# Performance work log

Measured on AMD Instinct MI355X. Metric: run time of the kernel, lower is better.

## Reference

```python
import jax, jax.numpy as jnp
import numpy as np

N_NODES = 100000
N_EDGES = 1600000
IN_DIM = 128
OUT_DIM = 32
N_HEADS = 4
NEG_SLOPE = 0.2  # DGL GATConv default LeakyReLU negative slope


def setup_inputs() -> dict:
    key = jax.random.key(0)
    k_h, k_src, k_dst, k_w, k_al, k_ar = jax.random.split(key, 6)
    h = jax.random.normal(k_h, (N_NODES, IN_DIM), dtype=jnp.float32)
    src = jax.random.randint(k_src, (N_EDGES,), 0, N_NODES, dtype=jnp.int32)
    dst = jnp.sort(jax.random.randint(k_dst, (N_EDGES,), 0, N_NODES, dtype=jnp.int32))
    # Xavier-ish init scale
    W = jax.random.normal(k_w, (IN_DIM, N_HEADS * OUT_DIM), dtype=jnp.float32) / np.sqrt(IN_DIM)
    attn_l = jax.random.normal(k_al, (N_HEADS, OUT_DIM), dtype=jnp.float32) / np.sqrt(OUT_DIM)
    attn_r = jax.random.normal(k_ar, (N_HEADS, OUT_DIM), dtype=jnp.float32) / np.sqrt(OUT_DIM)
    bias = jnp.zeros((N_HEADS * OUT_DIM,), dtype=jnp.float32)
    return {"h": h, "src": src, "dst": dst, "W": W, "attn_l": attn_l, "attn_r": attn_r, "bias": bias}


def reference(h, src, dst, W, attn_l, attn_r, bias):
    # Eval-mode GATConv (feat_drop / attn_drop disabled).
    N = h.shape[0]
    # Linear projection -> [N, H, D]
    feat = (h @ W).reshape(N, N_HEADS, OUT_DIM)
    # Per-node attention logits: el/er [N, H]
    el = jnp.einsum('nhd,hd->nh', feat, attn_l)
    er = jnp.einsum('nhd,hd->nh', feat, attn_r)
    # Edge scores: e = LeakyReLU(el[src] + er[dst])  -> [E, H]
    e = el[src] + er[dst]
    e = jnp.where(e > 0, e, NEG_SLOPE * e)
    # Segment softmax over incoming edges of each destination node
    e_max = jax.ops.segment_max(e, dst, num_segments=N, indices_are_sorted=True)
    e_exp = jnp.exp(e - e_max[dst])
    denom = jax.ops.segment_sum(e_exp, dst, num_segments=N, indices_are_sorted=True)
    alpha = e_exp / denom[dst]  # [E, H]
    # Weighted aggregate: sum_e alpha[e] * feat[src[e]] per destination
    msg = feat[src] * alpha[:, :, None]  # [E, H, D]
    rst = jax.ops.segment_sum(msg, dst, num_segments=N, indices_are_sorted=True)  # [N, H, D]
    # Bias + ReLU activation (GATLayer default activation=F.relu)
    rst = rst + bias.reshape(1, N_HEADS, OUT_DIM)
    return jax.nn.relu(rst)
```

## Files before the change

### kernel.cpp

```cpp
#include <hip/hip_runtime.h>
#include <hip/hip_fp16.h>
#include <math.h>

#define NEG_SLOPE 0.2f

typedef _Float16 f16x2 __attribute__((ext_vector_type(2)));
typedef _Float16 f16x8 __attribute__((ext_vector_type(8)));
typedef float f32x4 __attribute__((ext_vector_type(4)));

__device__ __forceinline__ float fdot2f(unsigned int a, unsigned int b, float c) {
#if __has_builtin(__builtin_amdgcn_fdot2)
    return __builtin_amdgcn_fdot2(__builtin_bit_cast(f16x2, a),
                                  __builtin_bit_cast(f16x2, b), c, false);
#else
    __half2 ah = __builtin_bit_cast(__half2, a), bh = __builtin_bit_cast(__half2, b);
    float2 af = __half22float2(ah), bf = __half22float2(bh);
    return c + af.x * bf.x + af.y * bf.y;
#endif
}

__device__ __forceinline__ unsigned int packw(float a, float b) {
#if __has_builtin(__builtin_amdgcn_cvt_pkrtz)
    return __builtin_bit_cast(unsigned int, __builtin_amdgcn_cvt_pkrtz(a, b));
#else
    return __builtin_bit_cast(unsigned int, __floats2half2_rn(a, b));
#endif
}

__global__ __launch_bounds__(256) void prep_seg_kernel(
    const float* __restrict__ W, __half* __restrict__ w16t,
    const int* __restrict__ dst, int* __restrict__ off, int E, int N)
{
    const int b = blockIdx.x;
    if (b < 64) {
        int tid = b * 256 + threadIdx.x;
        int c = tid >> 7, k = tid & 127;
        w16t[c * 128 + k] = __float2half(W[k * 128 + c]);
        return;
    }
    int i = (b - 64) * 256 + threadIdx.x;
    if (i >= E) return;
    int d = dst[i];
    int prev = (i == 0) ? -1 : dst[i - 1];
    for (int n = prev + 1; n <= d; ++n) off[n] = i;
    if (i == E - 1) {
        for (int n = d + 1; n <= N; ++n) off[n] = E;
    }
}

__global__ __launch_bounds__(256) void proj_kernel(
    const float* __restrict__ h, const __half* __restrict__ w16t,
    const float* __restrict__ attn_l, const float* __restrict__ attn_r,
    __half* __restrict__ feat, float* __restrict__ el, float* __restrict__ er,
    int N)
{
    __shared__ __half hl[64 * 128];
    __shared__ __half wl[128 * 128];
    const int t = threadIdx.x;
    const int nodeBase = blockIdx.x * 64;

#pragma unroll
    for (int i = 0; i < 8; ++i) {
        int ch = t + i * 256;
        int col = ch >> 4, k8 = ch & 15;
        uint4 v = *(const uint4*)(w16t + col * 128 + k8 * 8);
        int byte = col * 256 + k8 * 16;
        *(uint4*)((char*)wl + (byte ^ ((col & 7) << 4))) = v;
    }
#pragma unroll
    for (int i = 0; i < 8; ++i) {
        int slot = t + i * 256;
        int row = slot >> 5, c4 = slot & 31;
        int gn = nodeBase + row;
        float4 v = make_float4(0.f, 0.f, 0.f, 0.f);
        if (gn < N) v = *(const float4*)(h + (size_t)gn * 128 + c4 * 4);
        __half2 p0 = __floats2half2_rn(v.x, v.y);
        __half2 p1 = __floats2half2_rn(v.z, v.w);
        uint2 u = make_uint2(__builtin_bit_cast(unsigned int, p0),
                             __builtin_bit_cast(unsigned int, p1));
        int byte = row * 256 + c4 * 8;
        *(uint2*)((char*)hl + (byte ^ ((row & 7) << 4))) = u;
    }
    __syncthreads();

    const int l = t & 63, wave = t >> 6;
    const int arow = wave * 16 + (l & 15);
    const int kg = l >> 4;
    f32x4 acc[8];
#pragma unroll
    for (int i = 0; i < 8; ++i) acc[i] = (f32x4){0.f, 0.f, 0.f, 0.f};

#pragma unroll
    for (int kt = 0; kt < 4; ++kt) {
        const int kb = (kt * 32 + kg * 8) * 2;
        f16x8 a = *(const f16x8*)((const char*)hl +
                    ((arow * 256 + kb) ^ ((arow & 7) << 4)));
#pragma unroll
        for (int ct = 0; ct < 8; ++ct) {
            int bcol = ct * 16 + (l & 15);
            f16x8 b = *(const f16x8*)((const char*)wl +
                        ((bcol * 256 + kb) ^ ((bcol & 7) << 4)));
            acc[ct] = __builtin_amdgcn_mfma_f32_16x16x32_f16(a, b, acc[ct], 0, 0, 0);
        }
    }

    __syncthreads();
    const int colLo = l & 15;
    const int rowHi = wave * 16 + (l >> 4) * 4;
#pragma unroll
    for (int ct = 0; ct < 8; ++ct) {
#pragma unroll
        for (int r = 0; r < 4; ++r) {
            int row = rowHi + r;
            int byte = row * 256 + (ct * 16 + colLo) * 2;
            *(__half*)((char*)hl + (byte ^ ((row & 7) << 4))) = __float2half(acc[ct][r]);
        }
    }

    float pl[4][4], pr[4][4];
#pragma unroll
    for (int hh = 0; hh < 4; ++hh) {
        float al0 = attn_l[hh * 32 + colLo];
        float al1 = attn_l[hh * 32 + 16 + colLo];
        float ar0 = attn_r[hh * 32 + colLo];
        float ar1 = attn_r[hh * 32 + 16 + colLo];
#pragma unroll
        for (int r = 0; r < 4; ++r) {
            pl[hh][r] = acc[2 * hh][r] * al0 + acc[2 * hh + 1][r] * al1;
            pr[hh][r] = acc[2 * hh][r] * ar0 + acc[2 * hh + 1][r] * ar1;
        }
    }
#pragma unroll
    for (int msk = 1; msk <= 8; msk <<= 1) {
#pragma unroll
        for (int hh = 0; hh < 4; ++hh)
#pragma unroll
            for (int r = 0; r < 4; ++r) {
                pl[hh][r] += __shfl_xor(pl[hh][r], msk);
                pr[hh][r] += __shfl_xor(pr[hh][r], msk);
            }
    }
    if (colLo == 0) {
#pragma unroll
        for (int r = 0; r < 4; ++r) {
            int node = nodeBase + rowHi + r;
            if (node < N) {
                *(float4*)(el + (size_t)node * 4) =
                    make_float4(pl[0][r], pl[1][r], pl[2][r], pl[3][r]);
                *(float4*)(er + (size_t)node * 4) =
                    make_float4(pr[0][r], pr[1][r], pr[2][r], pr[3][r]);
            }
        }
    }
    __syncthreads();

    char* featB = (char*)feat + (size_t)nodeBase * 256;
#pragma unroll
    for (int i = 0; i < 4; ++i) {
        int c = t + i * 256;
        int row = c >> 4;
        uint4 v = *(const uint4*)((const char*)hl + ((c * 16) ^ ((row & 7) << 4)));
        if (nodeBase + row < N) *(uint4*)(featB + c * 16) = v;
    }
}

__global__ __launch_bounds__(256) void aggregate_kernel(
    const __half* __restrict__ feat, const float* __restrict__ el,
    const float* __restrict__ er, const int* __restrict__ off,
    const int* __restrict__ src, const float* __restrict__ bias,
    float* __restrict__ out, int N)
{
    const int wid = (int)((blockIdx.x * blockDim.x + threadIdx.x) >> 6);
    const int l = threadIdx.x & 63;
    if (wid >= N) return;
    const int n = __builtin_amdgcn_readfirstlane(wid);
    const int s = off[n];
    const int e = off[n + 1];
    const int f0 = 2 * l;
    const int hm = l >> 4;
    const float b0 = bias[f0], b1 = bias[f0 + 1];
    float* outp = out + (size_t)n * 128;
    if (s >= e) {
        outp[f0] = fmaxf(b0, 0.f);
        outp[f0 + 1] = fmaxf(b1, 0.f);
        return;
    }

    const float er_mine = er[n * 4 + hm];
    const float er_coop = er[n * 4 + (l & 3)];
    float ax = 0.f, ay = 0.f, dn = 0.f;
    const unsigned int one2 = 0x3C003C00u;

    int ei = s;
    for (; ei + 16 <= e; ei += 16) {
        int sv[16];
#pragma unroll
        for (int k = 0; k < 16; ++k) sv[k] = src[ei + k];
        int mysrc = src[ei + (l >> 2)];
        float sc = el[(size_t)mysrc * 4 + (l & 3)] + er_coop;
        sc = sc > 0.f ? sc : NEG_SLOPE * sc;
        float myw = __expf(sc);
        unsigned int g[16];
#pragma unroll
        for (int k = 0; k < 16; ++k)
            g[k] = *(const unsigned int*)(feat + (size_t)sv[k] * 128 + f0);
#pragma unroll
        for (int k = 0; k < 8; ++k) {
            float wa = __shfl(myw, 8 * k + hm);
            float wb = __shfl(myw, 8 * k + 4 + hm);
            unsigned int w2 = packw(wa, wb);
            unsigned int lo = __builtin_amdgcn_perm(g[2 * k + 1], g[2 * k], 0x05040100u);
            unsigned int hi = __builtin_amdgcn_perm(g[2 * k + 1], g[2 * k], 0x07060302u);
            ax = fdot2f(w2, lo, ax);
            ay = fdot2f(w2, hi, ay);
            dn = fdot2f(w2, one2, dn);
        }
    }
    if (ei + 8 <= e) {
        int sv[8];
#pragma unroll
        for (int k = 0; k < 8; ++k) sv[k] = src[ei + k];
        int mysrc = src[ei + ((l >> 2) & 7)];
        float sc = el[(size_t)mysrc * 4 + (l & 3)] + er_coop;
        sc = sc > 0.f ? sc : NEG_SLOPE * sc;
        float myw = __expf(sc);
        unsigned int g[8];
#pragma unroll
        for (int k = 0; k < 8; ++k)
            g[k] = *(const unsigned int*)(feat + (size_t)sv[k] * 128 + f0);
#pragma unroll
        for (int k = 0; k < 4; ++k) {
            float wa = __shfl(myw, 8 * k + hm);
            float wb = __shfl(myw, 8 * k + 4 + hm);
            unsigned int w2 = packw(wa, wb);
            unsigned int lo = __builtin_amdgcn_perm(g[2 * k + 1], g[2 * k], 0x05040100u);
            unsigned int hi = __builtin_amdgcn_perm(g[2 * k + 1], g[2 * k], 0x07060302u);
            ax = fdot2f(w2, lo, ax);
            ay = fdot2f(w2, hi, ay);
            dn = fdot2f(w2, one2, dn);
        }
        ei += 8;
    }
    if (ei + 4 <= e) {
        int sv0 = src[ei], sv1 = src[ei + 1], sv2 = src[ei + 2], sv3 = src[ei + 3];
        float e0 = el[(size_t)sv0 * 4 + hm], e1 = el[(size_t)sv1 * 4 + hm];
        float e2 = el[(size_t)sv2 * 4 + hm], e3 = el[(size_t)sv3 * 4 + hm];
        unsigned int g0 = *(const unsigned int*)(feat + (size_t)sv0 * 128 + f0);
        unsigned int g1 = *(const unsigned int*)(feat + (size_t)sv1 * 128 + f0);
        unsigned int g2 = *(const unsigned int*)(feat + (size_t)sv2 * 128 + f0);
        unsigned int g3 = *(const unsigned int*)(feat + (size_t)sv3 * 128 + f0);
        float s0 = e0 + er_mine, s1 = e1 + er_mine, s2 = e2 + er_mine, s3 = e3 + er_mine;
        s0 = s0 > 0.f ? s0 : NEG_SLOPE * s0;
        s1 = s1 > 0.f ? s1 : NEG_SLOPE * s1;
        s2 = s2 > 0.f ? s2 : NEG_SLOPE * s2;
        s3 = s3 > 0.f ? s3 : NEG_SLOPE * s3;
        unsigned int w2a = packw(__expf(s0), __expf(s1));
        unsigned int w2b = packw(__expf(s2), __expf(s3));
        unsigned int lo = __builtin_amdgcn_perm(g1, g0, 0x05040100u);
        unsigned int hi = __builtin_amdgcn_perm(g1, g0, 0x07060302u);
        ax = fdot2f(w2a, lo, ax); ay = fdot2f(w2a, hi, ay); dn = fdot2f(w2a, one2, dn);
        lo = __builtin_amdgcn_perm(g3, g2, 0x05040100u);
        hi = __builtin_amdgcn_perm(g3, g2, 0x07060302u);
        ax = fdot2f(w2b, lo, ax); ay = fdot2f(w2b, hi, ay); dn = fdot2f(w2b, one2, dn);
        ei += 4;
    }
    for (; ei < e; ++ei) {
        int sv = src[ei];
        float sc = el[(size_t)sv * 4 + hm] + er_mine;
        sc = sc > 0.f ? sc : NEG_SLOPE * sc;
        float w = __expf(sc);
        __half2 gh = *(const __half2*)(feat + (size_t)sv * 128 + f0);
        float2 fv = __half22float2(gh);
        ax += w * fv.x; ay += w * fv.y; dn += w;
    }
    const float inv = 1.f / dn;
    *(float2*)(outp + f0) = make_float2(fmaxf(ax * inv + b0, 0.f),
                                        fmaxf(ay * inv + b1, 0.f));
}

extern "C" void kernel_launch(void* const* d_in, const int* in_sizes, int n_in,
                              void* d_out, int out_size, void* d_ws, size_t ws_size,
                              hipStream_t stream)
{
    const float* h      = (const float*)d_in[0];
    const int*   src    = (const int*)d_in[1];
    const int*   dst    = (const int*)d_in[2];
    const float* W      = (const float*)d_in[3];
    const float* attn_l = (const float*)d_in[4];
    const float* attn_r = (const float*)d_in[5];
    const float* bias   = (const float*)d_in[6];
    const int N = in_sizes[0] / 128;
    const int E = in_sizes[1];
    float* out = (float*)d_out;

    char* ws = (char*)d_ws;
    __half* feat = (__half*)ws;            ws += (size_t)N * 128 * sizeof(__half);
    float*  el   = (float*)ws;             ws += (size_t)N * 4 * sizeof(float);
    float*  er   = (float*)ws;             ws += (size_t)N * 4 * sizeof(float);
    __half* w16t = (__half*)ws;            ws += 128 * 128 * sizeof(__half);
    int*    off  = (int*)ws;

    hipLaunchKernelGGL(prep_seg_kernel, dim3(64 + (E + 255) / 256), dim3(256), 0, stream,
                       W, w16t, dst, off, E, N);
    hipLaunchKernelGGL(proj_kernel, dim3((N + 63) / 64), dim3(256), 0, stream,
                       h, w16t, attn_l, attn_r, feat, el, er, N);
    hipLaunchKernelGGL(aggregate_kernel, dim3((N + 3) / 4), dim3(256), 0, stream,
                       feat, el, er, off, src, bias, out, N);
}
```

Before: 109.4 us.

## Double projection tile to 128 nodes and compute attention logits from LDS fp16 features

The projection kernel now uses 512 threads and 128 nodes per block, so each block amortises the load of the 32 KB weight tile over twice as many rows. The register-based attention-logit reduction with many cross-lane shuffles is replaced by a per-thread dot product over fp16 features read back from LDS, using fp16 copies of attn_l/attn_r prepared in the prep kernel. This removes shuffle overhead but computes el/er from fp16-rounded features, which slightly changes precision. It also raises LDS use to 64 KB per block, which may reduce how many blocks fit per CU.

```diff
diff --git a/kernel.cpp b/kernel.cpp
--- a/kernel.cpp
+++ b/kernel.cpp
@@ -29,6 +29,8 @@
 
 __global__ __launch_bounds__(256) void prep_seg_kernel(
     const float* __restrict__ W, __half* __restrict__ w16t,
+    const float* __restrict__ attn_l, const float* __restrict__ attn_r,
+    __half* __restrict__ al16, __half* __restrict__ ar16,
     const int* __restrict__ dst, int* __restrict__ off, int E, int N)
 {
     const int b = blockIdx.x;
@@ -36,6 +38,10 @@
         int tid = b * 256 + threadIdx.x;
         int c = tid >> 7, k = tid & 127;
         w16t[c * 128 + k] = __float2half(W[k * 128 + c]);
+        if (tid < 128) {
+            al16[tid] = __float2half(attn_l[tid]);
+            ar16[tid] = __float2half(attn_r[tid]);
+        }
         return;
     }
     int i = (b - 64) * 256 + threadIdx.x;
@@ -48,20 +54,20 @@
     }
 }
 
-__global__ __launch_bounds__(256) void proj_kernel(
+__global__ __launch_bounds__(512) void proj_kernel(
     const float* __restrict__ h, const __half* __restrict__ w16t,
-    const float* __restrict__ attn_l, const float* __restrict__ attn_r,
+    const __half* __restrict__ al16, const __half* __restrict__ ar16,
     __half* __restrict__ feat, float* __restrict__ el, float* __restrict__ er,
     int N)
 {
-    __shared__ __half hl[64 * 128];
+    __shared__ __half hl[128 * 128];
     __shared__ __half wl[128 * 128];
     const int t = threadIdx.x;
-    const int nodeBase = blockIdx.x * 64;
-
-#pragma unroll
-    for (int i = 0; i < 8; ++i) {
-        int ch = t + i * 256;
+    const int nodeBase = blockIdx.x * 128;
+
+#pragma unroll
+    for (int i = 0; i < 4; ++i) {
+        int ch = t + i * 512;
         int col = ch >> 4, k8 = ch & 15;
         uint4 v = *(const uint4*)(w16t + col * 128 + k8 * 8);
         int byte = col * 256 + k8 * 16;
@@ -69,7 +75,7 @@
     }
 #pragma unroll
     for (int i = 0; i < 8; ++i) {
-        int slot = t + i * 256;
+        int slot = t + i * 512;
         int row = slot >> 5, c4 = slot & 31;
         int gn = nodeBase + row;
         float4 v = make_float4(0.f, 0.f, 0.f, 0.f);
@@ -116,48 +122,33 @@
             *(__half*)((char*)hl + (byte ^ ((row & 7) << 4))) = __float2half(acc[ct][r]);
         }
     }
-
-    float pl[4][4], pr[4][4];
-#pragma unroll
-    for (int hh = 0; hh < 4; ++hh) {
-        float al0 = attn_l[hh * 32 + colLo];
-        float al1 = attn_l[hh * 32 + 16 + colLo];
-        float ar0 = attn_r[hh * 32 + colLo];
-        float ar1 = attn_r[hh * 32 + 16 + colLo];
-#pragma unroll
-        for (int r = 0; r < 4; ++r) {
-            pl[hh][r] = acc[2 * hh][r] * al0 + acc[2 * hh + 1][r] * al1;
-            pr[hh][r] = acc[2 * hh][r] * ar0 + acc[2 * hh + 1][r] * ar1;
-        }
-    }
-#pragma unroll
-    for (int msk = 1; msk <= 8; msk <<= 1) {
-#pragma unroll
-        for (int hh = 0; hh < 4; ++hh)
-#pragma unroll
-            for (int r = 0; r < 4; ++r) {
-                pl[hh][r] += __shfl_xor(pl[hh][r], msk);
-                pr[hh][r] += __shfl_xor(pr[hh][r], msk);
-            }
-    }
-    if (colLo == 0) {
-#pragma unroll
-        for (int r = 0; r < 4; ++r) {
-            int node = nodeBase + rowHi + r;
-            if (node < N) {
-                *(float4*)(el + (size_t)node * 4) =
-                    make_float4(pl[0][r], pl[1][r], pl[2][r], pl[3][r]);
-                *(float4*)(er + (size_t)node * 4) =
-                    make_float4(pr[0][r], pr[1][r], pr[2][r], pr[3][r]);
-            }
-        }
-    }
     __syncthreads();
 
+    {
+        const int row = t >> 2, head = t & 3;
+        const int node = nodeBase + row;
+        float lv = 0.f, rv = 0.f;
+#pragma unroll
+        for (int j = 0; j < 4; ++j) {
+            int byte = row * 256 + head * 64 + j * 16;
+            uint4 f = *(const uint4*)((const char*)hl + (byte ^ ((row & 7) << 4)));
+            uint4 a = *(const uint4*)(al16 + head * 32 + j * 8);
+            uint4 bb = *(const uint4*)(ar16 + head * 32 + j * 8);
+            lv = fdot2f(f.x, a.x, lv); rv = fdot2f(f.x, bb.x, rv);
+            lv = fdot2f(f.y, a.y, lv); rv = fdot2f(f.y, bb.y, rv);
+            lv = fdot2f(f.z, a.z, lv); rv = fdot2f(f.z, bb.z, rv);
+            lv = fdot2f(f.w, a.w, lv); rv = fdot2f(f.w, bb.w, rv);
+        }
+        if (node < N) {
+            el[(size_t)node * 4 + head] = lv;
+            er[(size_t)node * 4 + head] = rv;
+        }
+    }
+
     char* featB = (char*)feat + (size_t)nodeBase * 256;
 #pragma unroll
     for (int i = 0; i < 4; ++i) {
-        int c = t + i * 256;
+        int c = t + i * 512;
         int row = c >> 4;
         uint4 v = *(const uint4*)((const char*)hl + ((c * 16) ^ ((row & 7) << 4)));
         if (nodeBase + row < N) *(uint4*)(featB + c * 16) = v;
@@ -196,8 +187,8 @@
         int sv[16];
 #pragma unroll
         for (int k = 0; k < 16; ++k) sv[k] = src[ei + k];
-        int mysrc = src[ei + (l >> 2)];
-        float sc = el[(size_t)mysrc * 4 + (l & 3)] + er_coop;
+        int svc = src[ei + (l >> 2)];
+        float sc = el[(size_t)svc * 4 + (l & 3)] + er_coop;
         sc = sc > 0.f ? sc : NEG_SLOPE * sc;
         float myw = __expf(sc);
         unsigned int g[16];
@@ -220,8 +211,8 @@
         int sv[8];
 #pragma unroll
         for (int k = 0; k < 8; ++k) sv[k] = src[ei + k];
-        int mysrc = src[ei + ((l >> 2) & 7)];
-        float sc = el[(size_t)mysrc * 4 + (l & 3)] + er_coop;
+        int svc = src[ei + ((l >> 2) & 7)];
+        float sc = el[(size_t)svc * 4 + (l & 3)] + er_coop;
         sc = sc > 0.f ? sc : NEG_SLOPE * sc;
         float myw = __expf(sc);
         unsigned int g[8];
@@ -298,12 +289,14 @@
     float*  el   = (float*)ws;             ws += (size_t)N * 4 * sizeof(float);
     float*  er   = (float*)ws;             ws += (size_t)N * 4 * sizeof(float);
     __half* w16t = (__half*)ws;            ws += 128 * 128 * sizeof(__half);
+    __half* al16 = (__half*)ws;            ws += 256;
+    __half* ar16 = (__half*)ws;            ws += 256;
     int*    off  = (int*)ws;
 
     hipLaunchKernelGGL(prep_seg_kernel, dim3(64 + (E + 255) / 256), dim3(256), 0, stream,
-                       W, w16t, dst, off, E, N);
-    hipLaunchKernelGGL(proj_kernel, dim3((N + 63) / 64), dim3(256), 0, stream,
-                       h, w16t, attn_l, attn_r, feat, el, er, N);
+                       W, w16t, attn_l, attn_r, al16, ar16, dst, off, E, N);
+    hipLaunchKernelGGL(proj_kernel, dim3((N + 127) / 128), dim3(512), 0, stream,
+                       h, w16t, al16, ar16, feat, el, er, N);
     hipLaunchKernelGGL(aggregate_kernel, dim3((N + 3) / 4), dim3(256), 0, stream,
                        feat, el, er, off, src, bias, out, N);
 }
```

Result: faster. 103.3 us (-5.6%).
